# Optimization experiments

Measured on AMD Instinct MI355X. Metric: run time of the kernel, lower is better.

Reference implementation:

```python
import jax, jax.numpy as jnp
import numpy as np

DN = ('NCHW', 'OIHW', 'NCHW')
A, NC = 3, 80  # num_anchors, num_classes


def conv(x, w, b, pad=1):
    y = jax.lax.conv_general_dilated(x, w, (1, 1), [(pad, pad), (pad, pad)], dimension_numbers=DN)
    return y + b[None, :, None, None]


def up2(x):
    return jnp.repeat(jnp.repeat(x, 2, axis=2), 2, axis=3)


def gen_anchors():
    # AnchorGenerator: sizes per level, 3 aspect ratios, 1 scale, stride=2**(i+3)
    sizes = [32.0, 64.0, 128.0]
    ars = [0.5, 1.0, 2.0]
    hw = [(64, 64), (32, 32), (16, 16)]
    out = []
    for i, ((h, w), bs) in enumerate(zip(hw, sizes)):
        stride = 2.0 ** (i + 3)
        base = np.array([[-bs * np.sqrt(a) / 2, -bs / np.sqrt(a) / 2,
                          bs * np.sqrt(a) / 2, bs / np.sqrt(a) / 2] for a in ars], dtype=np.float32)
        sx = np.arange(w, dtype=np.float32) * stride
        sy = np.arange(h, dtype=np.float32) * stride
        yy, xx = np.meshgrid(sy, sx, indexing='ij')  # torch.meshgrid default 'ij'
        shifts = np.stack([xx.ravel(), yy.ravel(), xx.ravel(), yy.ravel()], axis=1)
        anc = (base[None, :, :] + shifts[:, None, :]).reshape(-1, 4)
        out.append(anc)
    return jnp.asarray(np.concatenate(out, axis=0))


def setup_inputs() -> dict:
    key = jax.random.key(0)
    ks = jax.random.split(key, 32)
    def w(k, o, i, kh, kw):
        return jax.random.normal(k, (o, i, kh, kw), jnp.float32) * 0.02
    B = 8
    inp = {
        'feat3': jax.random.normal(ks[0], (B, 512, 64, 64), jnp.float32),
        'feat4': jax.random.normal(ks[1], (B, 1024, 32, 32), jnp.float32),
        'feat5': jax.random.normal(ks[2], (B, 2048, 16, 16), jnp.float32),
        # FPN lateral 1x1 convs
        'lw0': w(ks[3], 256, 512, 1, 1),  'lb0': jnp.zeros(256, jnp.float32),
        'lw1': w(ks[4], 256, 1024, 1, 1), 'lb1': jnp.zeros(256, jnp.float32),
        'lw2': w(ks[5], 256, 2048, 1, 1), 'lb2': jnp.zeros(256, jnp.float32),
        # FPN 3x3 output convs
        'fw0': w(ks[6], 256, 256, 3, 3), 'fb0': jnp.zeros(256, jnp.float32),
        'fw1': w(ks[7], 256, 256, 3, 3), 'fb1': jnp.zeros(256, jnp.float32),
        'fw2': w(ks[8], 256, 256, 3, 3), 'fb2': jnp.zeros(256, jnp.float32),
        # cls tower (shared across levels)
        'cw0': w(ks[9], 256, 256, 3, 3),  'cb0': jnp.zeros(256, jnp.float32),
        'cw1': w(ks[10], 256, 256, 3, 3), 'cb1': jnp.zeros(256, jnp.float32),
        'cw2': w(ks[11], A * NC, 256, 3, 3), 'cb2': jnp.zeros(A * NC, jnp.float32),
        # reg tower (shared across levels)
        'rw0': w(ks[12], 256, 256, 3, 3), 'rb0': jnp.zeros(256, jnp.float32),
        'rw1': w(ks[13], 256, 256, 3, 3), 'rb1': jnp.zeros(256, jnp.float32),
        'rw2': w(ks[14], A * 4, 256, 3, 3), 'rb2': jnp.zeros(A * 4, jnp.float32),
    }
    return inp


def _tower(f, w0, b0, w1, b1, w2, b2):
    x = jax.nn.relu(conv(f, w0, b0))
    x = jax.nn.relu(conv(x, w1, b1))
    return conv(x, w2, b2)


def reference(feat3, feat4, feat5,
              lw0, lb0, lw1, lb1, lw2, lb2,
              fw0, fb0, fw1, fb1, fw2, fb2,
              cw0, cb0, cw1, cb1, cw2, cb2,
              rw0, rb0, rw1, rb1, rw2, rb2):
    B = feat3.shape[0]
    # FPN: lateral 1x1 convs + top-down nearest upsample fusion + 3x3 convs
    l0 = conv(feat3, lw0, lb0, pad=0)
    l1 = conv(feat4, lw1, lb1, pad=0)
    l2 = conv(feat5, lw2, lb2, pad=0)
    l1 = l1 + up2(l2)
    l0 = l0 + up2(l1)
    feats = [conv(l0, fw0, fb0), conv(l1, fw1, fb1), conv(l2, fw2, fb2)]
    cls_list, reg_list = [], []
    for f in feats:
        c = _tower(f, cw0, cb0, cw1, cb1, cw2, cb2)  # [B, A*NC, H, W]
        r = _tower(f, rw0, rb0, rw1, rb1, rw2, rb2)  # [B, A*4, H, W]
        H, W = c.shape[2], c.shape[3]
        # view(B, A, C, HW).permute(0, 3, 1, 2) -> [B, HW, A, C]
        c = c.reshape(B, A, NC, H * W).transpose(0, 3, 1, 2)
        r = r.reshape(B, A, 4, H * W).transpose(0, 3, 1, 2)
        cls_list.append(c.reshape(B, H * W, A * NC))
        reg_list.append(r.reshape(B, H * W, A * 4))
    cls_all = jnp.concatenate(cls_list, axis=1)   # [B, 5376, 240]
    reg_all = jnp.concatenate(reg_list, axis=1)   # [B, 5376, 12]
    out = jnp.concatenate([cls_all, reg_all], axis=-1)  # [B, 5376, 252]
    anchors = gen_anchors()  # [16128, 4]
    return out, anchors
```

## Files before the change

kernel.cpp:

```cpp
#include <hip/hip_runtime.h>

typedef __bf16 bf16_t;
typedef __bf16 bf16x8 __attribute__((ext_vector_type(8)));
typedef float f32x4 __attribute__((ext_vector_type(4)));

__device__ inline void gl_lds16(const bf16_t* g, bf16_t* l) {
  __builtin_amdgcn_global_load_lds(
      (const __attribute__((address_space(1))) void*)g,
      (__attribute__((address_space(3))) void*)l, 16, 0, 0);
}

__global__ __launch_bounds__(256)
void nchw_to_nhwc(const float* __restrict__ in, bf16_t* __restrict__ out,
                  int C, int HW) {
  __shared__ float tile[64][65];
  const int n = blockIdx.z;
  const int c0 = blockIdx.y * 64, p0 = blockIdx.x * 64;
  const int t = threadIdx.x;
  const float* src = in + ((size_t)n * C + c0) * HW + p0;
  const int cl = t >> 6;
  const int pl = t & 63;
#pragma unroll
  for (int i = 0; i < 16; ++i)
    tile[cl + i * 4][pl] = src[(size_t)(cl + i * 4) * HW + pl];
  __syncthreads();
  bf16_t* dst = out + ((size_t)n * HW + p0) * C + c0;
  const int pc = t >> 6;
  const int cc = t & 63;
#pragma unroll
  for (int i = 0; i < 16; ++i)
    dst[(size_t)(pc + i * 4) * C + cc] = (bf16_t)tile[cc][pc + i * 4];
}

struct WSrc {
  const float *lw0, *lw1, *lw2;
  const float* w9[9];
  int O9[9];
};
__global__ __launch_bounds__(256)
void weight_prep(WSrc s, bf16_t* __restrict__ LWT0, bf16_t* __restrict__ LWT1,
                 bf16_t* __restrict__ LWT2, bf16_t* __restrict__ W33) {
  int idx = blockIdx.x * 256 + threadIdx.x;
  if (idx < 131072) { LWT0[idx] = (bf16_t)s.lw0[idx]; return; }
  if (idx < 393216) { int i = idx - 131072; LWT1[i] = (bf16_t)s.lw1[i]; return; }
  if (idx < 917504) { int i = idx - 393216; LWT2[i] = (bf16_t)s.lw2[i]; return; }
  int t2 = idx - 917504;
  if (t2 >= 9 * 589824) return;
  int sgi = t2 / 589824;
  int r = t2 - sgi * 589824;
  int kid = r >> 16;
  int rem = r & 65535;
  int o = rem >> 8, ci = rem & 255;
  const float* src = s.w9[sgi];
  int O = s.O9[sgi];
  W33[t2] = (o < O) ? (bf16_t)src[((size_t)o * 256 + ci) * 9 + kid] : (bf16_t)0.0f;
}

__global__ __launch_bounds__(256)
void up2_add_p(bf16_t* __restrict__ dst, const bf16_t* __restrict__ src,
               int lw, int lhw, int dWp, int dNs, int sWp, int sNs, int tot8) {
  int idx = blockIdx.x * 256 + threadIdx.x;
  if (idx >= tot8) return;
  const int c8 = idx & 31;
  const int pos = idx >> 5;
  const int n = pos >> lhw;
  const int rem = pos & ((1 << lhw) - 1);
  const int y = rem >> lw, x = rem & ((1 << lw) - 1);
  bf16_t* d = dst + ((size_t)n * dNs + (y + 1) * dWp + (x + 1)) * 256 + c8 * 8;
  const bf16_t* sp = src + ((size_t)n * sNs + ((y >> 1) + 1) * sWp + ((x >> 1) + 1)) * 256 + c8 * 8;
  bf16x8 dv = *(bf16x8*)d;
  bf16x8 sv = *(const bf16x8*)sp;
#pragma unroll
  for (int k = 0; k < 8; ++k) dv[k] = (bf16_t)((float)dv[k] + (float)sv[k]);
  *(bf16x8*)d = dv;
}

struct Job1 {
  const bf16_t* A;
  const bf16_t* Wt;
  const float* bias;
  bf16_t* outb;
  int mtiles, lw, lhw, oWp, onstride, Cin, pad0, pad1;
};
struct Job1Pack { Job1 j[3]; };

__global__ __launch_bounds__(256, 2)
void conv1_batch(Job1Pack jp) {
  __shared__ __align__(16) bf16_t As[2][128 * 32];
  __shared__ __align__(16) bf16_t Bs[2][128 * 32];
  const int cpx = gridDim.x >> 3;
  int b = (blockIdx.x & 7) * cpx + (blockIdx.x >> 3);
  int ji = 0;
#pragma unroll 1
  for (; ji < 2; ++ji) {
    int sz = jp.j[ji].mtiles * 2;
    if (b < sz) break;
    b -= sz;
  }
  const Job1 J = jp.j[ji];
  const int nt = b & 1, mt = b >> 1;
  const int m0 = mt * 128, n0 = nt * 128;
  const int t = threadIdx.x, l = t & 63, w = t >> 6;
  const int W = 1 << J.lw, HW = 1 << J.lhw;
  const int sr = l >> 2, seg = (l & 3) * 8;
  const bf16_t* aptr[2];
  const bf16_t* bptr[2];
  int lrow[2];
#pragma unroll
  for (int q = 0; q < 2; ++q) {
    const int r = w * 32 + q * 16 + sr;
    aptr[q] = J.A + (size_t)(m0 + r) * J.Cin + seg;
    bptr[q] = J.Wt + (size_t)(n0 + r) * J.Cin + seg;
    lrow[q] = (w * 32 + q * 16) * 32;
  }
  const int fr = l & 15, qd = l >> 4;
  const int wm = (w & 1) * 64, wn = (w >> 1) * 64;

  f32x4 acc[4][4];
#pragma unroll
  for (int i = 0; i < 4; ++i)
#pragma unroll
    for (int j = 0; j < 4; ++j)
#pragma unroll
      for (int r = 0; r < 4; ++r) acc[i][j][r] = 0.0f;

  auto stage = [&](int buf, int kk) {
#pragma unroll
    for (int q = 0; q < 2; ++q) {
      gl_lds16(aptr[q] + (size_t)kk * 32, &As[buf][lrow[q]]);
      gl_lds16(bptr[q] + (size_t)kk * 32, &Bs[buf][lrow[q]]);
    }
  };

  stage(0, 0);

  const int kiters = J.Cin >> 5;
#pragma unroll 1
  for (int kk = 0; kk < kiters; ++kk) {
    const int cur = kk & 1;
    __syncthreads();
    if (kk + 1 < kiters) stage(cur ^ 1, kk + 1);
    bf16x8 af[4], bfv[4];
#pragma unroll
    for (int i = 0; i < 4; ++i)
      af[i] = *(const bf16x8*)&As[cur][(wm + i * 16 + fr) * 32 + qd * 8];
#pragma unroll
    for (int j = 0; j < 4; ++j)
      bfv[j] = *(const bf16x8*)&Bs[cur][(wn + j * 16 + fr) * 32 + qd * 8];
#pragma unroll
    for (int i = 0; i < 4; ++i)
#pragma unroll
      for (int j = 0; j < 4; ++j)
        acc[i][j] = __builtin_amdgcn_mfma_f32_16x16x32_bf16(af[i], bfv[j],
                                                            acc[i][j], 0, 0, 0);
  }

#pragma unroll
  for (int i = 0; i < 4; ++i) {
    const int mrow = m0 + wm + i * 16 + qd * 4;
#pragma unroll
    for (int j = 0; j < 4; ++j) {
      const int co = n0 + wn + j * 16 + fr;
      const float bv = J.bias[co];
#pragma unroll
      for (int r = 0; r < 4; ++r) {
        float v = acc[i][j][r] + bv;
        const int m = mrow + r;
        const int n = m >> J.lhw, hw = m & (HW - 1);
        const int y = hw >> J.lw, x = hw & (W - 1);
        J.outb[((size_t)n * J.onstride + (y + 1) * J.oWp + (x + 1)) * 256 + co] =
            (bf16_t)v;
      }
    }
  }
}

struct Job3 {
  const bf16_t* A;
  const bf16_t* Wt;
  const float* bias;
  bf16_t* outb;
  const bf16_t* Wt2;
  const float* bias2;
  bf16_t* outb2;
  int mtiles, ntiles, lw, lhw, Wp, nsA, oWp, onstride;
  int relu, Cout, pos_off, ch_off, use_outf, nAr, Pc, pad_;
};
struct Job3Pack { Job3 j[6]; };

__global__ __launch_bounds__(256, 3)
void conv3_batch(Job3Pack jp, float* __restrict__ outf) {
  __shared__ __align__(16) bf16_t As[320 * 32];
  __shared__ __align__(16) bf16_t Bs[384 * 32];
  const int cpx = gridDim.x >> 3;
  int b = (blockIdx.x & 7) * cpx + (blockIdx.x >> 3);
  int ji = 0;
#pragma unroll 1
  for (; ji < 5; ++ji) {
    int sz = jp.j[ji].mtiles * jp.j[ji].ntiles;
    if (b < sz) break;
    b -= sz;
  }
  const Job3 J = jp.j[ji];
  int s, mt;
  if (J.ntiles == 4)      { s = b & 3; mt = b >> 2; }
  else if (J.ntiles == 2) { s = b & 1; mt = b >> 1; }
  else                    { s = 0;     mt = b; }
  const int second = (s >= 2);
  const int n0 = (s & 1) * 128;
  const bf16_t* Wtp = second ? J.Wt2 : J.Wt;
  const float* biasp = second ? J.bias2 : J.bias;
  bf16_t* outbp = second ? J.outb2 : J.outb;
  const int m0 = mt * 128;
  const int t = threadIdx.x, l = t & 63, w = t >> 6;
  const int W = 1 << J.lw, HW = 1 << J.lhw;
  const int sr = l >> 2, seg = (l & 3) * 8;
  const int fr = l & 15, qd = l >> 4;
  const int wm = (w & 1) * 64, wn = (w >> 1) * 64;

  const int n_img = m0 >> J.lhw;
  const int Y0 = (m0 & (HW - 1)) >> J.lw;
  const bf16_t* Ag = J.A + ((size_t)n_img * J.nsA + (size_t)Y0 * J.Wp) * 256;

  int apix[4];
#pragma unroll
  for (int i = 0; i < 4; ++i) {
    const int m = wm + i * 16 + fr;
    const int y = m >> J.lw, x = m & (W - 1);
    apix[i] = ((y + 1) * J.Wp + (x + 1)) * 32 + qd * 8;
  }

  f32x4 acc[4][4];
#pragma unroll
  for (int i = 0; i < 4; ++i)
#pragma unroll
    for (int j = 0; j < 4; ++j)
#pragma unroll
      for (int r = 0; r < 4; ++r) acc[i][j][r] = 0.0f;

#pragma unroll 1
  for (int cb = 0; cb < 8; ++cb) {
    const int cboff = cb * 32;
#pragma unroll 1
    for (int ky = 0; ky < 3; ++ky) {
      __syncthreads();
#pragma unroll
      for (int r = 0; r < 6; ++r) {
        const int R = r * 64 + w * 16 + sr;
        const int tp = R >> 7, co = R & 127;
        gl_lds16(Wtp + (size_t)(ky * 3 + tp) * 65536 +
                     (size_t)(n0 + co) * 256 + cboff + seg,
                 &Bs[(r * 64 + w * 16) * 32]);
      }
      if (ky == 0) {
#pragma unroll 1
        for (int r = 0; r < J.nAr; ++r) {
          int p = r * 64 + w * 16 + sr;
          p = (p < J.Pc) ? p : (J.Pc - 1);
          gl_lds16(Ag + (size_t)p * 256 + cboff + seg,
                   &As[(r * 64 + w * 16) * 32]);
        }
      }
      __syncthreads();
      const int dyoff = (ky - 1) * J.Wp * 32;
#pragma unroll
      for (int kx = 0; kx < 3; ++kx) {
        const int d = dyoff + (kx - 1) * 32;
        bf16x8 af[4], bfv[4];
#pragma unroll
        for (int i = 0; i < 4; ++i)
          af[i] = *(const bf16x8*)&As[apix[i] + d];
#pragma unroll
        for (int j = 0; j < 4; ++j)
          bfv[j] = *(const bf16x8*)&Bs[(kx * 128 + wn + j * 16 + fr) * 32 + qd * 8];
#pragma unroll
        for (int i = 0; i < 4; ++i)
#pragma unroll
          for (int j = 0; j < 4; ++j)
            acc[i][j] = __builtin_amdgcn_mfma_f32_16x16x32_bf16(af[i], bfv[j],
                                                                acc[i][j], 0, 0, 0);
      }
    }
  }

#pragma unroll
  for (int i = 0; i < 4; ++i) {
    const int mrow = m0 + wm + i * 16 + qd * 4;
#pragma unroll
    for (int j = 0; j < 4; ++j) {
      const int co = n0 + wn + j * 16 + fr;
      if (co < J.Cout) {
        const float bv = biasp[co];
#pragma unroll
        for (int r = 0; r < 4; ++r) {
          float v = acc[i][j][r] + bv;
          if (J.relu) v = fmaxf(v, 0.0f);
          const int m = mrow + r;
          const int n = m >> J.lhw, hw = m & (HW - 1);
          if (J.use_outf) {
            outf[((size_t)n * 5376 + J.pos_off + hw) * 252 + J.ch_off + co] = v;
          } else {
            const int y = hw >> J.lw, x = hw & (W - 1);
            outbp[((size_t)n * J.onstride + (y + 1) * J.oWp + (x + 1)) * 256 + co] =
                (bf16_t)v;
          }
        }
      }
    }
  }
}

__global__ __launch_bounds__(256)
void anchors_k(float* __restrict__ out) {
  int r = blockIdx.x * 256 + threadIdx.x;
  if (r >= 16128) return;
  int local, w, stride;
  float bs;
  if (r < 12288)      { local = r;          w = 64; stride = 8;  bs = 32.f;  }
  else if (r < 15360) { local = r - 12288;  w = 32; stride = 16; bs = 64.f;  }
  else                { local = r - 15360;  w = 16; stride = 32; bs = 128.f; }
  const int a = local % 3;
  const int s = local / 3;
  const int y = s / w, x = s - y * w;
  const float ar = (a == 0) ? 0.5f : (a == 1) ? 1.0f : 2.0f;
  const float sq = sqrtf(ar);
  const float hw_ = bs * sq * 0.5f, hh = bs / sq * 0.5f;
  const float cx = (float)x * (float)stride, cy = (float)y * (float)stride;
  out[(size_t)r * 4 + 0] = cx - hw_;
  out[(size_t)r * 4 + 1] = cy - hh;
  out[(size_t)r * 4 + 2] = cx + hw_;
  out[(size_t)r * 4 + 3] = cy + hh;
}

extern "C" void kernel_launch(void* const* d_in, const int* in_sizes, int n_in,
                              void* d_out, int out_size, void* d_ws, size_t ws_size,
                              hipStream_t stream) {
  const float* feat3 = (const float*)d_in[0];
  const float* feat4 = (const float*)d_in[1];
  const float* feat5 = (const float*)d_in[2];
  const float* lw0 = (const float*)d_in[3];  const float* lb0 = (const float*)d_in[4];
  const float* lw1 = (const float*)d_in[5];  const float* lb1 = (const float*)d_in[6];
  const float* lw2 = (const float*)d_in[7];  const float* lb2 = (const float*)d_in[8];
  const float* fw0 = (const float*)d_in[9];  const float* fb0 = (const float*)d_in[10];
  const float* fw1 = (const float*)d_in[11]; const float* fb1 = (const float*)d_in[12];
  const float* fw2 = (const float*)d_in[13]; const float* fb2 = (const float*)d_in[14];
  const float* cw0 = (const float*)d_in[15]; const float* cb0 = (const float*)d_in[16];
  const float* cw1 = (const float*)d_in[17]; const float* cb1 = (const float*)d_in[18];
  const float* cw2 = (const float*)d_in[19]; const float* cb2 = (const float*)d_in[20];
  const float* rw0 = (const float*)d_in[21]; const float* rb0 = (const float*)d_in[22];
  const float* rw1 = (const float*)d_in[23]; const float* rb1 = (const float*)d_in[24];
  const float* rw2 = (const float*)d_in[25]; const float* rb2 = (const float*)d_in[26];

  char* ws = (char*)d_ws;
  float* out = (float*)d_out;

  bf16_t* XS3 = (bf16_t*)(ws + 0);
  bf16_t* XS4 = (bf16_t*)(ws + 33554432);
  bf16_t* XS5 = (bf16_t*)(ws + 50331648);
  bf16_t* Lp0 = (bf16_t*)(ws + 58720256);
  bf16_t* Lp1 = (bf16_t*)(ws + 76562432);
  bf16_t* Lp2 = (bf16_t*)(ws + 81297408);
  bf16_t* Pp0 = (bf16_t*)(ws + 82624512);
  bf16_t* Pp1 = (bf16_t*)(ws + 100466688);
  bf16_t* Pp2 = (bf16_t*)(ws + 105201664);
  bf16_t* LWT0 = (bf16_t*)(ws + 106528768);
  bf16_t* LWT1 = (bf16_t*)(ws + 106790912);
  bf16_t* LWT2 = (bf16_t*)(ws + 107315200);
  bf16_t* W33  = (bf16_t*)(ws + 108363776);
  bf16_t* FWT0 = W33 + 0 * 589824;
  bf16_t* FWT1 = W33 + 1 * 589824;
  bf16_t* FWT2 = W33 + 2 * 589824;
  bf16_t* CWT0 = W33 + 3 * 589824;
  bf16_t* CWT1 = W33 + 4 * 589824;
  bf16_t* CWT2 = W33 + 5 * 589824;
  bf16_t* RWT0 = W33 + 6 * 589824;
  bf16_t* RWT1 = W33 + 7 * 589824;
  bf16_t* RWT2 = W33 + 8 * 589824;
  bf16_t* TAc0 = (bf16_t*)(ws + 0);
  bf16_t* TAr0 = (bf16_t*)(ws + 17842176);
  bf16_t* TAc1 = (bf16_t*)(ws + 35684352);
  bf16_t* TAr1 = (bf16_t*)(ws + 40419328);
  bf16_t* TAc2 = (bf16_t*)(ws + 45154304);
  bf16_t* TAr2 = (bf16_t*)(ws + 46481408);
  bf16_t* TBc0 = Pp0; bf16_t* TBr0 = Lp0;
  bf16_t* TBc1 = Pp1; bf16_t* TBr1 = Lp1;
  bf16_t* TBc2 = Pp2; bf16_t* TBr2 = Lp2;

  WSrc wsrc;
  wsrc.lw0 = lw0; wsrc.lw1 = lw1; wsrc.lw2 = lw2;
  const float* w9s[9] = {fw0, fw1, fw2, cw0, cw1, cw2, rw0, rw1, rw2};
  int o9s[9] = {256, 256, 256, 256, 256, 240, 256, 256, 12};
  for (int i = 0; i < 9; ++i) { wsrc.w9[i] = w9s[i]; wsrc.O9[i] = o9s[i]; }
  weight_prep<<<dim3(24320), 256, 0, stream>>>(wsrc, LWT0, LWT1, LWT2, W33);

  nchw_to_nhwc<<<dim3(64, 8, 8),  256, 0, stream>>>(feat3, XS3, 512, 4096);
  nchw_to_nhwc<<<dim3(16, 16, 8), 256, 0, stream>>>(feat4, XS4, 1024, 1024);
  nchw_to_nhwc<<<dim3(4, 32, 8),  256, 0, stream>>>(feat5, XS5, 2048, 256);

  hipMemsetAsync(ws + 58720256, 0, 47808512, stream);

  {
    Job1Pack jp;
    jp.j[0] = {XS3, LWT0, lb0, Lp0, 256, 6, 12, 66, 4356, 512, 0, 0};
    jp.j[1] = {XS4, LWT1, lb1, Lp1, 64, 5, 10, 34, 1156, 1024, 0, 0};
    jp.j[2] = {XS5, LWT2, lb2, Lp2, 16, 4, 8, 18, 324, 2048, 0, 0};
    conv1_batch<<<dim3(672), 256, 0, stream>>>(jp);
  }

  hipMemsetAsync(ws + 0, 0, 47808512, stream);

  up2_add_p<<<dim3(1024), 256, 0, stream>>>(Lp1, Lp2, 5, 10, 34, 1156, 18, 324, 262144);
  up2_add_p<<<dim3(4096), 256, 0, stream>>>(Lp0, Lp1, 6, 12, 66, 4356, 34, 1156, 1048576);

  auto mk3 = [](const bf16_t* A, const bf16_t* Wt, const float* bias,
                bf16_t* outb, int mtiles, int ntiles, int lw, int lhw,
                int Wp, int nsA, int oWp, int onstride, int relu, int Cout,
                int pos_off, int ch_off, int use_outf, int nAr, int Pc) {
    Job3 j;
    j.A = A; j.Wt = Wt; j.bias = bias; j.outb = outb;
    j.Wt2 = Wt; j.bias2 = bias; j.outb2 = outb;
    j.mtiles = mtiles; j.ntiles = ntiles; j.lw = lw; j.lhw = lhw;
    j.Wp = Wp; j.nsA = nsA; j.oWp = oWp; j.onstride = onstride;
    j.relu = relu; j.Cout = Cout; j.pos_off = pos_off; j.ch_off = ch_off;
    j.use_outf = use_outf; j.nAr = nAr; j.Pc = Pc; j.pad_ = 0;
    return j;
  };

  {
    Job3Pack jp;
    jp.j[0] = mk3(Lp0, FWT0, fb0, Pp0, 256, 2, 6, 12, 66, 4356, 66, 4356, 0, 256, 0, 0, 0, 5, 264);
    jp.j[1] = mk3(Lp1, FWT1, fb1, Pp1, 64, 2, 5, 10, 34, 1156, 34, 1156, 0, 256, 0, 0, 0, 4, 204);
    jp.j[2] = mk3(Lp2, FWT2, fb2, Pp2, 16, 2, 4, 8, 18, 324, 18, 324, 0, 256, 0, 0, 0, 3, 180);
    jp.j[3] = jp.j[4] = jp.j[5] = jp.j[2];
    jp.j[3].mtiles = jp.j[4].mtiles = jp.j[5].mtiles = 0;
    conv3_batch<<<dim3(672), 256, 0, stream>>>(jp, out);
  }

  {
    Job3Pack jp;
    jp.j[0] = mk3(Pp0, CWT0, cb0, TAc0, 256, 4, 6, 12, 66, 4356, 66, 4356, 1, 256, 0, 0, 0, 5, 264);
    jp.j[0].Wt2 = RWT0; jp.j[0].bias2 = rb0; jp.j[0].outb2 = TAr0;
    jp.j[1] = mk3(Pp1, CWT0, cb0, TAc1, 64, 4, 5, 10, 34, 1156, 34, 1156, 1, 256, 0, 0, 0, 4, 204);
    jp.j[1].Wt2 = RWT0; jp.j[1].bias2 = rb0; jp.j[1].outb2 = TAr1;
    jp.j[2] = mk3(Pp2, CWT0, cb0, TAc2, 16, 4, 4, 8, 18, 324, 18, 324, 1, 256, 0, 0, 0, 3, 180);
    jp.j[2].Wt2 = RWT0; jp.j[2].bias2 = rb0; jp.j[2].outb2 = TAr2;
    jp.j[3] = jp.j[4] = jp.j[5] = jp.j[2];
    jp.j[3].mtiles = jp.j[4].mtiles = jp.j[5].mtiles = 0;
    conv3_batch<<<dim3(1344), 256, 0, stream>>>(jp, out);
  }

  {
    Job3Pack jp;
    jp.j[0] = mk3(TAc0, CWT1, cb1, TBc0, 256, 2, 6, 12, 66, 4356, 66, 4356, 1, 256, 0, 0, 0, 5, 264);
    jp.j[1] = mk3(TAr0, RWT1, rb1, TBr0, 256, 2, 6, 12, 66, 4356, 66, 4356, 1, 256, 0, 0, 0, 5, 264);
    jp.j[2] = mk3(TAc1, CWT1, cb1, TBc1, 64, 2, 5, 10, 34, 1156, 34, 1156, 1, 256, 0, 0, 0, 4, 204);
    jp.j[3] = mk3(TAr1, RWT1, rb1, TBr1, 64, 2, 5, 10, 34, 1156, 34, 1156, 1, 256, 0, 0, 0, 4, 204);
    jp.j[4] = mk3(TAc2, CWT1, cb1, TBc2, 16, 2, 4, 8, 18, 324, 18, 324, 1, 256, 0, 0, 0, 3, 180);
    jp.j[5] = mk3(TAr2, RWT1, rb1, TBr2, 16, 2, 4, 8, 18, 324, 18, 324, 1, 256, 0, 0, 0, 3, 180);
    conv3_batch<<<dim3(1344), 256, 0, stream>>>(jp, out);
  }

  {
    Job3Pack jp;
    jp.j[0] = mk3(TBc0, CWT2, cb2, nullptr, 256, 2, 6, 12, 66, 4356, 0, 0, 0, 240, 0, 0, 1, 5, 264);
    jp.j[1] = mk3(TBr0, RWT2, rb2, nullptr, 256, 1, 6, 12, 66, 4356, 0, 0, 0, 12, 0, 240, 1, 5, 264);
    jp.j[2] = mk3(TBc1, CWT2, cb2, nullptr, 64, 2, 5, 10, 34, 1156, 0, 0, 0, 240, 4096, 0, 1, 4, 204);
    jp.j[3] = mk3(TBr1, RWT2, rb2, nullptr, 64, 1, 5, 10, 34, 1156, 0, 0, 0, 12, 4096, 240, 1, 4, 204);
    jp.j[4] = mk3(TBc2, CWT2, cb2, nullptr, 16, 2, 4, 8, 18, 324, 0, 0, 0, 240, 5120, 0, 1, 3, 180);
    jp.j[5] = mk3(TBr2, RWT2, rb2, nullptr, 16, 1, 4, 8, 18, 324, 0, 0, 0, 12, 5120, 240, 1, 3, 180);
    conv3_batch<<<dim3(1008), 256, 0, stream>>>(jp, out);
  }

  anchors_k<<<dim3(63), 256, 0, stream>>>(out + 10838016);
}
```

Measured before the change: 674.1 us.

## Zero only padded borders, single-buffer conv1, add narrow-N path for reg head

Two full-buffer memsets are replaced with a kernel that zeroes only the one-pixel halo ring of each padded activation buffer, removing most of the memset traffic. conv1_batch drops its LDS double buffering in favour of a synchronous load-sync-compute loop, which reduces shared memory and may raise occupancy but exposes load latency. The final 12-channel regression conv gets a dedicated path using 256-row M tiles and a single 16-wide N fragment, so it no longer computes a padded 128-wide output tile. The grid is resized to match. Correctness depends on interiors being fully overwritten before they are read.

```diff
diff --git a/kernel.cpp b/kernel.cpp
--- a/kernel.cpp
+++ b/kernel.cpp
@@ -56,6 +56,37 @@
   W33[t2] = (o < O) ? (bf16_t)src[((size_t)o * 256 + ci) * 9 + kid] : (bf16_t)0.0f;
 }
 
+struct BZJob { bf16_t* p; int Wp, Hp, nsA, ringN, count; };
+struct BZPack { BZJob j[6]; };
+__global__ __launch_bounds__(256)
+void zero_borders(BZPack bp) {
+  int idx = blockIdx.x * 256 + threadIdx.x;
+  int ji = 0;
+#pragma unroll 1
+  for (; ji < 5; ++ji) {
+    if (idx < bp.j[ji].count) break;
+    idx -= bp.j[ji].count;
+  }
+  const BZJob J = bp.j[ji];
+  if (idx >= J.count) return;
+  const int c8 = idx & 31;
+  const int rp = idx >> 5;
+  const int n = rp / J.ringN;
+  const int r = rp - n * J.ringN;
+  int y, x;
+  if (r < J.Wp)          { y = 0;         x = r; }
+  else if (r < 2 * J.Wp) { y = J.Hp - 1;  x = r - J.Wp; }
+  else {
+    const int rr = r - 2 * J.Wp;
+    y = 1 + (rr >> 1);
+    x = (rr & 1) ? (J.Wp - 1) : 0;
+  }
+  bf16x8 z;
+#pragma unroll
+  for (int k = 0; k < 8; ++k) z[k] = (bf16_t)0.0f;
+  *(bf16x8*)&J.p[((size_t)n * J.nsA + y * J.Wp + x) * 256 + c8 * 8] = z;
+}
+
 __global__ __launch_bounds__(256)
 void up2_add_p(bf16_t* __restrict__ dst, const bf16_t* __restrict__ src,
                int lw, int lhw, int dWp, int dNs, int sWp, int sNs, int tot8) {
@@ -86,8 +117,8 @@
 
 __global__ __launch_bounds__(256, 2)
 void conv1_batch(Job1Pack jp) {
-  __shared__ __align__(16) bf16_t As[2][128 * 32];
-  __shared__ __align__(16) bf16_t Bs[2][128 * 32];
+  __shared__ __align__(16) bf16_t As[128 * 32];
+  __shared__ __align__(16) bf16_t Bs[128 * 32];
   const int cpx = gridDim.x >> 3;
   int b = (blockIdx.x & 7) * cpx + (blockIdx.x >> 3);
   int ji = 0;
@@ -105,13 +136,15 @@
   const int sr = l >> 2, seg = (l & 3) * 8;
   const bf16_t* aptr[2];
   const bf16_t* bptr[2];
-  int lrow[2];
+  bf16_t* alds[2];
+  bf16_t* blds[2];
 #pragma unroll
   for (int q = 0; q < 2; ++q) {
     const int r = w * 32 + q * 16 + sr;
     aptr[q] = J.A + (size_t)(m0 + r) * J.Cin + seg;
+    alds[q] = &As[(w * 32 + q * 16) * 32];
     bptr[q] = J.Wt + (size_t)(n0 + r) * J.Cin + seg;
-    lrow[q] = (w * 32 + q * 16) * 32;
+    blds[q] = &Bs[(w * 32 + q * 16) * 32];
   }
   const int fr = l & 15, qd = l >> 4;
   const int wm = (w & 1) * 64, wn = (w >> 1) * 64;
@@ -124,29 +157,23 @@
 #pragma unroll
       for (int r = 0; r < 4; ++r) acc[i][j][r] = 0.0f;
 
-  auto stage = [&](int buf, int kk) {
-#pragma unroll
-    for (int q = 0; q < 2; ++q) {
-      gl_lds16(aptr[q] + (size_t)kk * 32, &As[buf][lrow[q]]);
-      gl_lds16(bptr[q] + (size_t)kk * 32, &Bs[buf][lrow[q]]);
-    }
-  };
-
-  stage(0, 0);
-
   const int kiters = J.Cin >> 5;
 #pragma unroll 1
   for (int kk = 0; kk < kiters; ++kk) {
-    const int cur = kk & 1;
     __syncthreads();
-    if (kk + 1 < kiters) stage(cur ^ 1, kk + 1);
+    gl_lds16(aptr[0], alds[0]);
+    gl_lds16(aptr[1], alds[1]);
+    gl_lds16(bptr[0], blds[0]);
+    gl_lds16(bptr[1], blds[1]);
+    __syncthreads();
+    aptr[0] += 32; aptr[1] += 32; bptr[0] += 32; bptr[1] += 32;
     bf16x8 af[4], bfv[4];
 #pragma unroll
     for (int i = 0; i < 4; ++i)
-      af[i] = *(const bf16x8*)&As[cur][(wm + i * 16 + fr) * 32 + qd * 8];
+      af[i] = *(const bf16x8*)&As[(wm + i * 16 + fr) * 32 + qd * 8];
 #pragma unroll
     for (int j = 0; j < 4; ++j)
-      bfv[j] = *(const bf16x8*)&Bs[cur][(wn + j * 16 + fr) * 32 + qd * 8];
+      bfv[j] = *(const bf16x8*)&Bs[(wn + j * 16 + fr) * 32 + qd * 8];
 #pragma unroll
     for (int i = 0; i < 4; ++i)
 #pragma unroll
@@ -190,7 +217,7 @@
 
 __global__ __launch_bounds__(256, 3)
 void conv3_batch(Job3Pack jp, float* __restrict__ outf) {
-  __shared__ __align__(16) bf16_t As[320 * 32];
+  __shared__ __align__(16) bf16_t As[448 * 32];
   __shared__ __align__(16) bf16_t Bs[384 * 32];
   const int cpx = gridDim.x >> 3;
   int b = (blockIdx.x & 7) * cpx + (blockIdx.x >> 3);
@@ -211,11 +238,84 @@
   const bf16_t* Wtp = second ? J.Wt2 : J.Wt;
   const float* biasp = second ? J.bias2 : J.bias;
   bf16_t* outbp = second ? J.outb2 : J.outb;
-  const int m0 = mt * 128;
   const int t = threadIdx.x, l = t & 63, w = t >> 6;
   const int W = 1 << J.lw, HW = 1 << J.lhw;
   const int sr = l >> 2, seg = (l & 3) * 8;
   const int fr = l & 15, qd = l >> 4;
+
+  if (J.pad_) {
+    const int m0 = mt * 256;
+    const int n_img = m0 >> J.lhw;
+    const int Y0 = (m0 & (HW - 1)) >> J.lw;
+    const bf16_t* Ag = J.A + ((size_t)n_img * J.nsA + (size_t)Y0 * J.Wp) * 256;
+    int apix[4];
+#pragma unroll
+    for (int i = 0; i < 4; ++i) {
+      const int m = w * 64 + i * 16 + fr;
+      const int y = m >> J.lw, x = m & (W - 1);
+      apix[i] = ((y + 1) * J.Wp + (x + 1)) * 32 + qd * 8;
+    }
+    f32x4 acc[4];
+#pragma unroll
+    for (int i = 0; i < 4; ++i)
+#pragma unroll
+      for (int r = 0; r < 4; ++r) acc[i][r] = 0.0f;
+
+#pragma unroll 1
+    for (int cb = 0; cb < 8; ++cb) {
+      const int cboff = cb * 32;
+#pragma unroll 1
+      for (int ky = 0; ky < 3; ++ky) {
+        __syncthreads();
+        if (w < 3) {
+          gl_lds16(Wtp + (size_t)(ky * 3 + w) * 65536 +
+                       (size_t)(l >> 2) * 256 + cboff + (l & 3) * 8,
+                   &Bs[w * 512]);
+        }
+        if (ky == 0) {
+#pragma unroll 1
+          for (int r = 0; r < J.nAr; ++r) {
+            int p = r * 64 + w * 16 + sr;
+            p = (p < J.Pc) ? p : (J.Pc - 1);
+            gl_lds16(Ag + (size_t)p * 256 + cboff + seg,
+                     &As[(r * 64 + w * 16) * 32]);
+          }
+        }
+        __syncthreads();
+        const int dyoff = (ky - 1) * J.Wp * 32;
+#pragma unroll
+        for (int kx = 0; kx < 3; ++kx) {
+          const int d = dyoff + (kx - 1) * 32;
+          bf16x8 bfv = *(const bf16x8*)&Bs[kx * 512 + fr * 32 + qd * 8];
+#pragma unroll
+          for (int i = 0; i < 4; ++i) {
+            bf16x8 af = *(const bf16x8*)&As[apix[i] + d];
+            acc[i] = __builtin_amdgcn_mfma_f32_16x16x32_bf16(af, bfv,
+                                                             acc[i], 0, 0, 0);
+          }
+        }
+      }
+    }
+    const int co = fr;
+    if (co < J.Cout) {
+      const float bv = biasp[co];
+#pragma unroll
+      for (int i = 0; i < 4; ++i) {
+        const int mrow = m0 + w * 64 + i * 16 + qd * 4;
+#pragma unroll
+        for (int r = 0; r < 4; ++r) {
+          float v = acc[i][r] + bv;
+          if (J.relu) v = fmaxf(v, 0.0f);
+          const int m = mrow + r;
+          const int n = m >> J.lhw, hw = m & (HW - 1);
+          outf[((size_t)n * 5376 + J.pos_off + hw) * 252 + J.ch_off + co] = v;
+        }
+      }
+    }
+    return;
+  }
+
+  const int m0 = mt * 128;
   const int wm = (w & 1) * 64, wn = (w >> 1) * 64;
 
   const int n_img = m0 >> J.lhw;
@@ -397,7 +497,16 @@
   nchw_to_nhwc<<<dim3(16, 16, 8), 256, 0, stream>>>(feat4, XS4, 1024, 1024);
   nchw_to_nhwc<<<dim3(4, 32, 8),  256, 0, stream>>>(feat5, XS5, 2048, 256);
 
-  hipMemsetAsync(ws + 58720256, 0, 47808512, stream);
+  {
+    BZPack bp;
+    bp.j[0] = {Lp0, 66, 66, 4356, 260, 66560};
+    bp.j[1] = {Lp1, 34, 34, 1156, 132, 33792};
+    bp.j[2] = {Lp2, 18, 18, 324,  68,  17408};
+    bp.j[3] = {Pp0, 66, 66, 4356, 260, 66560};
+    bp.j[4] = {Pp1, 34, 34, 1156, 132, 33792};
+    bp.j[5] = {Pp2, 18, 18, 324,  68,  17408};
+    zero_borders<<<dim3(920), 256, 0, stream>>>(bp);
+  }
 
   {
     Job1Pack jp;
@@ -407,7 +516,16 @@
     conv1_batch<<<dim3(672), 256, 0, stream>>>(jp);
   }
 
-  hipMemsetAsync(ws + 0, 0, 47808512, stream);
+  {
+    BZPack bp;
+    bp.j[0] = {TAc0, 66, 66, 4356, 260, 66560};
+    bp.j[1] = {TAr0, 66, 66, 4356, 260, 66560};
+    bp.j[2] = {TAc1, 34, 34, 1156, 132, 33792};
+    bp.j[3] = {TAr1, 34, 34, 1156, 132, 33792};
+    bp.j[4] = {TAc2, 18, 18, 324,  68,  17408};
+    bp.j[5] = {TAr2, 18, 18, 324,  68,  17408};
+    zero_borders<<<dim3(920), 256, 0, stream>>>(bp);
+  }
 
   up2_add_p<<<dim3(1024), 256, 0, stream>>>(Lp1, Lp2, 5, 10, 34, 1156, 18, 324, 262144);
   up2_add_p<<<dim3(4096), 256, 0, stream>>>(Lp0, Lp1, 6, 12, 66, 4356, 34, 1156, 1048576);
@@ -462,13 +580,16 @@
 
   {
     Job3Pack jp;
-    jp.j[0] = mk3(TBc0, CWT2, cb2, nullptr, 256, 2, 6, 12, 66, 4356, 0, 0, 0, 240, 0, 0, 1, 5, 264);
-    jp.j[1] = mk3(TBr0, RWT2, rb2, nullptr, 256, 1, 6, 12, 66, 4356, 0, 0, 0, 12, 0, 240, 1, 5, 264);
+    jp.j[0] = mk3(TBc0, CWT2, cb2, nullptr, 512 / 2, 2, 6, 12, 66, 4356, 0, 0, 0, 240, 0, 0, 1, 5, 264);
+    jp.j[1] = mk3(TBr0, RWT2, rb2, nullptr, 128, 1, 6, 12, 66, 4356, 0, 0, 0, 12, 0, 240, 1, 7, 396);
+    jp.j[1].pad_ = 1;
     jp.j[2] = mk3(TBc1, CWT2, cb2, nullptr, 64, 2, 5, 10, 34, 1156, 0, 0, 0, 240, 4096, 0, 1, 4, 204);
-    jp.j[3] = mk3(TBr1, RWT2, rb2, nullptr, 64, 1, 5, 10, 34, 1156, 0, 0, 0, 12, 4096, 240, 1, 4, 204);
+    jp.j[3] = mk3(TBr1, RWT2, rb2, nullptr, 32, 1, 5, 10, 34, 1156, 0, 0, 0, 12, 4096, 240, 1, 6, 340);
+    jp.j[3].pad_ = 1;
     jp.j[4] = mk3(TBc2, CWT2, cb2, nullptr, 16, 2, 4, 8, 18, 324, 0, 0, 0, 240, 5120, 0, 1, 3, 180);
-    jp.j[5] = mk3(TBr2, RWT2, rb2, nullptr, 16, 1, 4, 8, 18, 324, 0, 0, 0, 12, 5120, 240, 1, 3, 180);
-    conv3_batch<<<dim3(1008), 256, 0, stream>>>(jp, out);
+    jp.j[5] = mk3(TBr2, RWT2, rb2, nullptr, 8, 1, 4, 8, 18, 324, 0, 0, 0, 12, 5120, 240, 1, 6, 324);
+    jp.j[5].pad_ = 1;
+    conv3_batch<<<dim3(840), 256, 0, stream>>>(jp, out);
   }
 
   anchors_k<<<dim3(63), 256, 0, stream>>>(out + 10838016);
```

After: 648.4 us. 1.04x faster.
